# Performance work log

Hardware: AMD Instinct MI355X
Metric: run time of the kernel (lower is better)

The kernel has to match this reference:

```python
import jax, jax.numpy as jnp
import numpy as np

P = 512        # number of graph pairs
MAXN = 192     # max(len_s) by construction
D_IN = 32      # num_input_features
HID = 64       # hidden_dim
REG = 0.1      # entropic reg
ITERS = 8      # numItermax in forward call
DEG = 8        # avg degree for synthetic edges


def setup_inputs() -> dict:
    key = jax.random.key(0)
    ks = jax.random.split(key, 16)
    len_s = np.asarray(96 + (np.arange(P) % 97), dtype=np.int32)          # 96..192
    len_t = np.asarray(32 + ((np.arange(P) * 7) % 65), dtype=np.int32)    # 32..96 <= len_s
    Ns, Nt = int(len_s.sum()), int(len_t.sum())
    return {
        "x_s": jax.random.normal(ks[0], (Ns, D_IN), jnp.float32),
        "x_t": jax.random.normal(ks[1], (Nt, D_IN), jnp.float32),
        "W_rel0": 0.1 * jax.random.normal(ks[2], (D_IN, HID), jnp.float32),
        "b_rel0": 0.1 * jax.random.normal(ks[3], (HID,), jnp.float32),
        "W_root0": 0.1 * jax.random.normal(ks[4], (D_IN, HID), jnp.float32),
        "W_rel1": 0.1 * jax.random.normal(ks[5], (HID, HID), jnp.float32),
        "b_rel1": 0.1 * jax.random.normal(ks[6], (HID,), jnp.float32),
        "W_root1": 0.1 * jax.random.normal(ks[7], (HID, HID), jnp.float32),
        "W_e": 0.1 * jax.random.normal(ks[8], (D_IN + 2 * HID, 64), jnp.float32),
        "b_e": 0.1 * jax.random.normal(ks[9], (64,), jnp.float32),
        "virtual": jax.random.uniform(ks[10], (64,), jnp.float32),
        "edge_index_s": jax.random.randint(ks[11], (2, Ns * DEG), 0, Ns, dtype=jnp.int32),
        "edge_index_t": jax.random.randint(ks[12], (2, Nt * DEG), 0, Nt, dtype=jnp.int32),
        "len_s": jnp.asarray(len_s),
        "len_t": jnp.asarray(len_t),
    }


def _normalize(x):
    return x / jnp.clip(jnp.linalg.norm(x, axis=-1, keepdims=True), 1e-12)


def _gnn_embed(x, ei, layers, W_e, b_e):
    # GraphConv: out = lin_rel(sum_{j->i} x_j) + lin_root(x_i), then relu; cat all layer outputs
    outs = [x]
    h = x
    for (Wr, br, Wo) in layers:
        agg = jax.ops.segment_sum(h[ei[0]], ei[1], num_segments=h.shape[0])
        h = jax.nn.relu(agg @ Wr + br + h @ Wo)
        outs.append(h)
    emb = jnp.concatenate(outs, axis=1) @ W_e + b_e
    return _normalize(emb)


def _pad_gather(emb, lens):
    # [total, E] -> [P, MAXN, E] via per-pair offsets (indices clipped; invalid masked later)
    off = jnp.cumsum(lens) - lens
    idx = jnp.clip(off[:, None] + jnp.arange(MAXN)[None, :], 0, emb.shape[0] - 1)
    return emb[idx]


def reference(x_s, x_t, W_rel0, b_rel0, W_root0, W_rel1, b_rel1, W_root1,
              W_e, b_e, virtual, edge_index_s, edge_index_t, len_s, len_t):
    layers = [(W_rel0, b_rel0, W_root0), (W_rel1, b_rel1, W_root1)]
    emb_s = _gnn_embed(x_s, edge_index_s, layers, W_e, b_e)  # [Ns, 64]
    emb_t = _gnn_embed(x_t, edge_index_t, layers, W_e, b_e)  # [Nt, 64]
    virt = _normalize(virtual[None, :])[0]

    s_pad = _pad_gather(emb_s, len_s)  # [P, MAXN, 64]
    t_pad = _pad_gather(emb_t, len_t)  # [P, MAXN, 64]
    j = jnp.arange(MAXN)
    # columns >= len_t use the virtual node embedding (covers j in [m, n))
    t_mask = (j[None, :] < len_t[:, None])[:, :, None]
    t_aug = jnp.where(t_mask, t_pad, virt[None, None, :])

    # Euclidean cdist via quadratic expansion
    sq_s = jnp.sum(s_pad * s_pad, -1)                              # [P, MAXN]
    sq_t = jnp.sum(t_aug * t_aug, -1)                              # [P, MAXN]
    dot = jnp.einsum('pid,pjd->pij', s_pad, t_aug)                 # [P, MAXN, MAXN]
    cd = jnp.sqrt(jnp.maximum(sq_s[:, :, None] + sq_t[:, None, :] - 2.0 * dot, 1e-12))

    # padded cost: real block = cdist, bottom-right pad block = 0, rest = 1000
    row_valid = j[None, :] < len_s[:, None]                        # [P, MAXN] (n = len_s)
    in_block = row_valid[:, :, None] & row_valid[:, None, :]
    pad_block = (~row_valid)[:, :, None] & (~row_valid)[:, None, :]
    cost = jnp.where(in_block, cd, jnp.where(pad_block, 0.0, 1000.0))

    # Sinkhorn-Knopp, a = b = ones(MAXN) so Kp = K and updates are 1/(K v), 1/(K^T u)
    K = jnp.exp(-cost / REG)

    def body(_, uv):
        u, v = uv
        v = 1.0 / jnp.einsum('pij,pi->pj', K, u)
        u = 1.0 / jnp.einsum('pij,pj->pi', K, v)
        return (u, v)

    u0 = jnp.full((P, MAXN), 1.0 / MAXN, dtype=cost.dtype)
    u, v = jax.lax.fori_loop(0, ITERS, body, (u0, u0))
    gamma = jax.lax.stop_gradient(u[:, :, None] * K * v[:, None, :])

    geds = jnp.sum(gamma * cost, axis=(1, 2))
    geds2 = geds / (len_s + len_t).astype(cost.dtype)
    return gamma, cost, geds2
```

## Files before the change

kernel.cpp:

```cpp
#include <hip/hip_runtime.h>
#include <math.h>

#define PAIRS 512
#define MAXN 192

#define LDS_BAR() asm volatile("s_waitcnt lgkmcnt(0)\n\ts_barrier" ::: "memory")

__global__ void offsets_kernel(const int* __restrict__ ls, const int* __restrict__ lt,
                               int* __restrict__ off) {
    __shared__ int wa[8], wb[8];
    int t = threadIdx.x;
    int a = ls[t], b = lt[t];
    int ia = a, ib = b;
#pragma unroll
    for (int d = 1; d < 64; d <<= 1) {
        int xa = __shfl_up(ia, d, 64);
        int xb = __shfl_up(ib, d, 64);
        if ((t & 63) >= d) { ia += xa; ib += xb; }
    }
    if ((t & 63) == 63) { wa[t >> 6] = ia; wb[t >> 6] = ib; }
    __syncthreads();
    int pa = 0, pb = 0;
    for (int w = 0; w < (t >> 6); w++) { pa += wa[w]; pb += wb[w]; }
    off[t] = pa + ia - a;
    off[PAIRS + t] = pb + ib - b;
}

__global__ __launch_bounds__(256) void count2_kernel(const int* __restrict__ eiS,
                                                     const int* __restrict__ eiT,
                                                     int* __restrict__ cnt,
                                                     int Es, int Et, int split) {
    int e = blockIdx.x * 256 + threadIdx.x;
    if (e < Es) atomicAdd(&cnt[eiS[Es + e]], 1);
    else if (e < Es + Et) atomicAdd(&cnt[split + eiT[Et + (e - Es)]], 1);
}

__global__ __launch_bounds__(256) void scan1_kernel(int* __restrict__ data,
                                                    int* __restrict__ blockSums, int N) {
    __shared__ int sc[256];
    int t = threadIdx.x;
    int base = blockIdx.x * 1024;
    int v[4];
    int s = 0;
#pragma unroll
    for (int q = 0; q < 4; q++) {
        int i = base + t * 4 + q;
        v[q] = (i < N) ? data[i] : 0;
        s += v[q];
    }
    sc[t] = s;
    __syncthreads();
    for (int d = 1; d < 256; d <<= 1) {
        int x = (t >= d) ? sc[t - d] : 0;
        __syncthreads();
        sc[t] += x;
        __syncthreads();
    }
    int excl = sc[t] - s;
#pragma unroll
    for (int q = 0; q < 4; q++) {
        int i = base + t * 4 + q;
        if (i < N) { data[i] = excl; excl += v[q]; }
    }
    if (t == 255) blockSums[blockIdx.x] = sc[255];
}

__global__ void scan2_kernel(int* __restrict__ blockSums, int B) {
    __shared__ int sh[256];
    int t = threadIdx.x;
    int v = (t < B) ? blockSums[t] : 0;
    sh[t] = v;
    __syncthreads();
    for (int d = 1; d < 256; d <<= 1) {
        int x = (t >= d) ? sh[t - d] : 0;
        __syncthreads();
        sh[t] += x;
        __syncthreads();
    }
    if (t < B) blockSums[t] = sh[t] - v;
}

__global__ __launch_bounds__(256) void scan3_kernel(int* __restrict__ data,
                                                    const int* __restrict__ blockSums,
                                                    int* __restrict__ cursor, int N) {
    int i = blockIdx.x * 256 + threadIdx.x;
    if (i < N) {
        int v = data[i] + blockSums[i >> 10];
        data[i] = v;
        cursor[i] = v;
    }
}

__global__ __launch_bounds__(256) void fill2_kernel(const int* __restrict__ eiS,
                                                    const int* __restrict__ eiT,
                                                    int* __restrict__ cursor,
                                                    int* __restrict__ src,
                                                    int Es, int Et, int split) {
    int e = blockIdx.x * 256 + threadIdx.x;
    if (e < Es) {
        int p = atomicAdd(&cursor[eiS[Es + e]], 1);
        src[p] = eiS[e];
    } else if (e < Es + Et) {
        int ee = e - Es;
        int p = atomicAdd(&cursor[split + eiT[Et + ee]], 1);
        src[p] = eiT[ee];
    }
}

template <int F>
__global__ __launch_bounds__(256) void gather_kernel(const float* __restrict__ featA,
                                                     const float* __restrict__ featB,
                                                     int split,
                                                     const int* __restrict__ rs,
                                                     const int* __restrict__ re,
                                                     const int* __restrict__ src,
                                                     float* __restrict__ agg, int N) {
    int gid = blockIdx.x * 256 + threadIdx.x;
    int row = gid / F;
    int lane = threadIdx.x & (F - 1);
    if (row >= N) return;
    int b = rs[row], e = re[row];
    int cnt = e - b;
    const float* feat = (row < split) ? featA : featB;
    int pre = cnt < F ? cnt : F;
    int sidx = (lane < cnt) ? src[b + lane] : 0;
    float acc = 0.f;
    for (int q = 0; q < pre; q++) {
        int s = __shfl(sidx, q, F);
        acc += feat[(size_t)s * F + lane];
    }
    for (int q = b + F; q < e; q++) acc += feat[(size_t)src[q] * F + lane];
    agg[(size_t)row * F + lane] = acc;
}


#define FMA_ROW(r, av)                                     \
    acc[r][0] = fmaf(av.x, w0.x, acc[r][0]);               \
    acc[r][1] = fmaf(av.x, w0.y, acc[r][1]);               \
    acc[r][2] = fmaf(av.x, w0.z, acc[r][2]);               \
    acc[r][3] = fmaf(av.x, w0.w, acc[r][3]);               \
    acc[r][0] = fmaf(av.y, w1.x, acc[r][0]);               \
    acc[r][1] = fmaf(av.y, w1.y, acc[r][1]);               \
    acc[r][2] = fmaf(av.y, w1.z, acc[r][2]);               \
    acc[r][3] = fmaf(av.y, w1.w, acc[r][3]);               \
    acc[r][0] = fmaf(av.z, w2.x, acc[r][0]);               \
    acc[r][1] = fmaf(av.z, w2.y, acc[r][1]);               \
    acc[r][2] = fmaf(av.z, w2.z, acc[r][2]);               \
    acc[r][3] = fmaf(av.z, w2.w, acc[r][3]);               \
    acc[r][0] = fmaf(av.w, w3.x, acc[r][0]);               \
    acc[r][1] = fmaf(av.w, w3.y, acc[r][1]);               \
    acc[r][2] = fmaf(av.w, w3.z, acc[r][2]);               \
    acc[r][3] = fmaf(av.w, w3.w, acc[r][3]);

#define GEMM_INNER(KW4, AKP, WBP)                                          \
    _Pragma("unroll") for (int k4 = 0; k4 < (KW4); k4++) {                 \
        float4 a0 = *(const float4*)((AKP) + (i)      * 68 + 4 * k4);      \
        float4 a1 = *(const float4*)((AKP) + (i + 16) * 68 + 4 * k4);      \
        float4 a2 = *(const float4*)((AKP) + (i + 32) * 68 + 4 * k4);      \
        float4 a3 = *(const float4*)((AKP) + (i + 48) * 68 + 4 * k4);      \
        float4 w0 = (WBP)[(4 * k4 + 0) * 16 + j];                          \
        float4 w1 = (WBP)[(4 * k4 + 1) * 16 + j];                          \
        float4 w2 = (WBP)[(4 * k4 + 2) * 16 + j];                          \
        float4 w3 = (WBP)[(4 * k4 + 3) * 16 + j];                          \
        FMA_ROW(0, a0) FMA_ROW(1, a1) FMA_ROW(2, a2) FMA_ROW(3, a3)        \
    }

template <int KIN>
__global__ __launch_bounds__(256) void lin_gemm_kernel(const float* __restrict__ agg,
    const float* __restrict__ hinA, const float* __restrict__ hinB, int split,
    const float* __restrict__ Wrel, const float* __restrict__ brel,
    const float* __restrict__ Wroot, float* __restrict__ hout, int N) {
    __shared__ float Abuf[64 * 68];
    __shared__ float4 Wbuf[64 * 16];
    int tid = threadIdx.x;
    int i = tid & 15, j = tid >> 4;
    int rowbase = blockIdx.x * 64;
    float4 bv = ((const float4*)brel)[j];
    float acc[4][4];
#pragma unroll
    for (int r = 0; r < 4; r++) { acc[r][0] = bv.x; acc[r][1] = bv.y; acc[r][2] = bv.z; acc[r][3] = bv.w; }

    for (int c0 = 0; c0 < 2 * KIN; c0 += 64) {
        __syncthreads();
        for (int t = tid; t < 1024; t += 256) {
            int k4 = t & 15, r = t >> 4;
            int kg = c0 + 4 * k4;
            int row = rowbase + r; if (row >= N) row = N - 1;
            float4 v;
            if (kg < KIN) {
                v = ((const float4*)(agg + (size_t)row * KIN))[kg >> 2];
            } else {
                int kk = kg - KIN;
                const float* h = (row < split) ? hinA + (size_t)row * KIN
                                               : hinB + (size_t)(row - split) * KIN;
                v = ((const float4*)h)[kk >> 2];
            }
            *(float4*)(Abuf + r * 68 + 4 * k4) = v;
        }
        for (int t = tid; t < 1024; t += 256) {
            int k = t >> 4, jj = t & 15;
            int kg = c0 + k;
            const float* Wsrc = (kg < KIN) ? (Wrel + (size_t)kg * 64)
                                           : (Wroot + (size_t)(kg - KIN) * 64);
            Wbuf[t] = ((const float4*)Wsrc)[jj];
        }
        __syncthreads();
        GEMM_INNER(16, Abuf, Wbuf)
    }
#pragma unroll
    for (int r = 0; r < 4; r++) {
        int row = rowbase + i + 16 * r;
        if (row < N) {
            float4 o = make_float4(fmaxf(acc[r][0], 0.f), fmaxf(acc[r][1], 0.f),
                                   fmaxf(acc[r][2], 0.f), fmaxf(acc[r][3], 0.f));
            ((float4*)(hout + (size_t)row * 64))[j] = o;
        }
    }
}

__global__ __launch_bounds__(256) void lin64_emb_kernel(
    const float* __restrict__ agg, const float* __restrict__ h1,
    const float* __restrict__ xA, const float* __restrict__ xB, int split,
    const float* __restrict__ Wrel, const float* __restrict__ brel,
    const float* __restrict__ Wroot,
    const float* __restrict__ We, const float* __restrict__ be,
    float* __restrict__ emb, int N) {
    __shared__ float Abuf[64 * 68];
    __shared__ float4 Wbuf[64 * 16];
    __shared__ float h2buf[64 * 68];
    int tid = threadIdx.x;
    int i = tid & 15, j = tid >> 4;
    int rowbase = blockIdx.x * 64;

    {
        float4 bv = ((const float4*)brel)[j];
        float acc[4][4];
#pragma unroll
        for (int r = 0; r < 4; r++) { acc[r][0] = bv.x; acc[r][1] = bv.y; acc[r][2] = bv.z; acc[r][3] = bv.w; }

        for (int c0 = 0; c0 < 128; c0 += 64) {
            __syncthreads();
            for (int t = tid; t < 1024; t += 256) {
                int k4 = t & 15, r = t >> 4;
                int kg = c0 + 4 * k4;
                int row = rowbase + r; if (row >= N) row = N - 1;
                float4 v;
                if (kg < 64) v = ((const float4*)(agg + (size_t)row * 64))[kg >> 2];
                else         v = ((const float4*)(h1 + (size_t)row * 64))[(kg - 64) >> 2];
                *(float4*)(Abuf + r * 68 + 4 * k4) = v;
            }
            for (int t = tid; t < 1024; t += 256) {
                int k = t >> 4, jj = t & 15;
                int kg = c0 + k;
                const float* Wsrc = (kg < 64) ? (Wrel + (size_t)kg * 64)
                                              : (Wroot + (size_t)(kg - 64) * 64);
                Wbuf[t] = ((const float4*)Wsrc)[jj];
            }
            __syncthreads();
            GEMM_INNER(16, Abuf, Wbuf)
        }
#pragma unroll
        for (int r = 0; r < 4; r++) {
            float4 o = make_float4(fmaxf(acc[r][0], 0.f), fmaxf(acc[r][1], 0.f),
                                   fmaxf(acc[r][2], 0.f), fmaxf(acc[r][3], 0.f));
            *(float4*)(h2buf + (i + 16 * r) * 68 + 4 * j) = o;
        }
    }

    float4 bv = ((const float4*)be)[j];
    float acc[4][4];
#pragma unroll
    for (int r = 0; r < 4; r++) { acc[r][0] = bv.x; acc[r][1] = bv.y; acc[r][2] = bv.z; acc[r][3] = bv.w; }

    __syncthreads();
    for (int t = tid; t < 1024; t += 256) {
        int k4 = t & 15, r = t >> 4;
        int kg = 4 * k4;
        int row = rowbase + r; if (row >= N) row = N - 1;
        float4 v;
        if (kg < 32) {
            const float* x = (row < split) ? xA + (size_t)row * 32
                                           : xB + (size_t)(row - split) * 32;
            v = ((const float4*)x)[kg >> 2];
        } else {
            v = ((const float4*)(h1 + (size_t)row * 64))[(kg - 32) >> 2];
        }
        *(float4*)(Abuf + r * 68 + 4 * k4) = v;
    }
    for (int t = tid; t < 1024; t += 256) {
        int k = t >> 4, jj = t & 15;
        Wbuf[t] = ((const float4*)(We + (size_t)k * 64))[jj];
    }
    __syncthreads();
    GEMM_INNER(16, Abuf, Wbuf)

    __syncthreads();
    for (int t = tid; t < 512; t += 256) {
        int k4 = t & 7, r = t >> 3;
        int row = rowbase + r; if (row >= N) row = N - 1;
        float4 v = ((const float4*)(h1 + (size_t)row * 64))[8 + k4];
        *(float4*)(Abuf + r * 68 + 4 * k4) = v;
    }
    for (int t = tid; t < 512; t += 256) {
        int k = t >> 4, jj = t & 15;
        Wbuf[t] = ((const float4*)(We + (size_t)(64 + k) * 64))[jj];
    }
    __syncthreads();
    GEMM_INNER(8, Abuf, Wbuf)

    __syncthreads();
    for (int t = tid; t < 1024; t += 256) {
        int k = t >> 4, jj = t & 15;
        Wbuf[t] = ((const float4*)(We + (size_t)(96 + k) * 64))[jj];
    }
    __syncthreads();
    GEMM_INNER(16, h2buf, Wbuf)

    __syncthreads();
#pragma unroll
    for (int r = 0; r < 4; r++)
#pragma unroll
        for (int c = 0; c < 4; c++)
            Abuf[(i + 16 * r) * 68 + 4 * j + c] = acc[r][c];
    __syncthreads();
    int lane = tid & 63, wv = tid >> 6;
    for (int rr = 0; rr < 16; rr++) {
        int r = wv * 16 + rr;
        float val = Abuf[r * 68 + lane];
        float ss = val * val;
#pragma unroll
        for (int d = 32; d > 0; d >>= 1) ss += __shfl_xor(ss, d, 64);
        int row = rowbase + r;
        if (row < N) emb[(size_t)row * 64 + lane] = val / fmaxf(sqrtf(ss), 1e-12f);
    }
}

__device__ __forceinline__ void dot_half(float kh[3][12], const float* sS, const float* sT,
                                         int ti, int tj) {
#pragma unroll
    for (int s = 0; s < 3; s++)
#pragma unroll
        for (int b = 0; b < 12; b++) kh[s][b] = 0.f;
    for (int k4 = 0; k4 < 16; k4++) {
        float4 a0 = *(const float4*)(sS + (3 * ti + 0) * 68 + 4 * k4);
        float4 a1 = *(const float4*)(sS + (3 * ti + 1) * 68 + 4 * k4);
        float4 a2 = *(const float4*)(sS + (3 * ti + 2) * 68 + 4 * k4);
#pragma unroll
        for (int b = 0; b < 12; b++) {
            float4 tb = *(const float4*)(sT + (12 * tj + b) * 68 + 4 * k4);
            kh[0][b] = fmaf(a0.x, tb.x, kh[0][b]);
            kh[0][b] = fmaf(a0.y, tb.y, kh[0][b]);
            kh[0][b] = fmaf(a0.z, tb.z, kh[0][b]);
            kh[0][b] = fmaf(a0.w, tb.w, kh[0][b]);
            kh[1][b] = fmaf(a1.x, tb.x, kh[1][b]);
            kh[1][b] = fmaf(a1.y, tb.y, kh[1][b]);
            kh[1][b] = fmaf(a1.z, tb.z, kh[1][b]);
            kh[1][b] = fmaf(a1.w, tb.w, kh[1][b]);
            kh[2][b] = fmaf(a2.x, tb.x, kh[2][b]);
            kh[2][b] = fmaf(a2.y, tb.y, kh[2][b]);
            kh[2][b] = fmaf(a2.z, tb.z, kh[2][b]);
            kh[2][b] = fmaf(a2.w, tb.w, kh[2][b]);
        }
    }
}

__device__ __forceinline__ void epi_half(float kh[3][12], const float* sqS, const float* sqT,
                                         int h, int ti, int tj, int n, int p,
                                         float* __restrict__ cost_out) {
#pragma unroll
    for (int s = 0; s < 3; s++) {
        int i = 96 * h + 3 * ti + s;
        bool rv = i < n;
        float sqi = sqS[3 * ti + s];
        float tmp[12];
#pragma unroll
        for (int b = 0; b < 12; b++) {
            int j = 12 * tj + b;
            float cd = sqrtf(fmaxf(sqi + sqT[j] - 2.f * kh[s][b], 1e-12f));
            float c = (rv && (j < n)) ? cd : ((!rv && (j >= n)) ? 0.f : 1000.f);
            tmp[b] = c;
            kh[s][b] = __expf(-10.f * c);
        }
        float* orow = cost_out + ((size_t)p * MAXN + i) * MAXN + 12 * tj;
#pragma unroll
        for (int q = 0; q < 3; q++)
            ((float4*)orow)[q] = make_float4(tmp[4 * q], tmp[4 * q + 1],
                                             tmp[4 * q + 2], tmp[4 * q + 3]);
    }
}

__global__ __launch_bounds__(512, 4) void fused_cost_sinkhorn_kernel(
    const float* __restrict__ embS, const float* __restrict__ embT,
    const float* __restrict__ vraw,
    const int* __restrict__ lenS, const int* __restrict__ lenT,
    const int* __restrict__ off,
    float* __restrict__ cost_out, float* __restrict__ gamma_out,
    float* __restrict__ geds2, int Ns) {
    __shared__ __align__(16) float sT[192 * 68];
    __shared__ __align__(16) float sS[96 * 68];
    __shared__ __align__(16) float sqT[192];
    __shared__ __align__(16) float sqS[96];
    __shared__ __align__(16) float virtv[64];

    int p = blockIdx.x;
    int tid = threadIdx.x;
    int ti = tid & 31;
    int tj = tid >> 5;
    int n = lenS[p], m = lenT[p];
    int offs = off[p], offt = off[PAIRS + p];

    if (tid < 64) {
        float v = vraw[tid];
        float ss = v * v;
#pragma unroll
        for (int d = 32; d > 0; d >>= 1) ss += __shfl_xor(ss, d, 64);
        virtv[tid] = v / fmaxf(sqrtf(ss), 1e-12f);
    }
    __syncthreads();

    for (int t = tid; t < 192 * 16; t += 512) {
        int j = t >> 4, q = t & 15;
        float4 vv = (j < m) ? ((const float4*)embT)[(size_t)(offt + j) * 16 + q]
                            : ((const float4*)virtv)[q];
        *(float4*)(sT + j * 68 + 4 * q) = vv;
    }
    for (int t = tid; t < 96 * 16; t += 512) {
        int r = t >> 4, q = t & 15;
        int gi = offs + r; if (gi > Ns - 1) gi = Ns - 1;
        float4 vv = ((const float4*)embS)[(size_t)gi * 16 + q];
        *(float4*)(sS + r * 68 + 4 * q) = vv;
    }
    __syncthreads();
    if (tid < 192) {
        float s = 0.f;
#pragma unroll
        for (int k = 0; k < 64; k++) { float a = sT[tid * 68 + k]; s = fmaf(a, a, s); }
        sqT[tid] = s;
    } else if (tid < 288) {
        int r = tid - 192;
        float s = 0.f;
#pragma unroll
        for (int k = 0; k < 64; k++) { float a = sS[r * 68 + k]; s = fmaf(a, a, s); }
        sqS[r] = s;
    }
    __syncthreads();

    float kf[2][3][12];

    dot_half(kf[0], sS, sT, ti, tj);
    float4 pf0, pf1, pf2;
    {
        int t0 = tid, t1 = tid + 512, t2 = tid + 1024;
        int gi0 = offs + 96 + (t0 >> 4); if (gi0 > Ns - 1) gi0 = Ns - 1;
        int gi1 = offs + 96 + (t1 >> 4); if (gi1 > Ns - 1) gi1 = Ns - 1;
        int gi2 = offs + 96 + (t2 >> 4); if (gi2 > Ns - 1) gi2 = Ns - 1;
        pf0 = ((const float4*)embS)[(size_t)gi0 * 16 + (t0 & 15)];
        pf1 = ((const float4*)embS)[(size_t)gi1 * 16 + (t1 & 15)];
        pf2 = ((const float4*)embS)[(size_t)gi2 * 16 + (t2 & 15)];
    }
    epi_half(kf[0], sqS, sqT, 0, ti, tj, n, p, cost_out);

    LDS_BAR();
    {
        int t0 = tid, t1 = tid + 512, t2 = tid + 1024;
        *(float4*)(sS + (t0 >> 4) * 68 + 4 * (t0 & 15)) = pf0;
        *(float4*)(sS + (t1 >> 4) * 68 + 4 * (t1 & 15)) = pf1;
        *(float4*)(sS + (t2 >> 4) * 68 + 4 * (t2 & 15)) = pf2;
    }
    LDS_BAR();
    if (tid < 96) {
        float s = 0.f;
#pragma unroll
        for (int k = 0; k < 64; k++) { float a = sS[tid * 68 + k]; s = fmaf(a, a, s); }
        sqS[tid] = s;
    }
    LDS_BAR();

    dot_half(kf[1], sS, sT, ti, tj);
    epi_half(kf[1], sqS, sqT, 1, ti, tj, n, p, cost_out);
    LDS_BAR();

    float* part = sS;
    float* ubuf = sS + 6336;
    float* vbuf = sqT;

    if (tid < 192) ubuf[tid] = 1.f / 192.f;
    LDS_BAR();

    for (int it = 0; it < 8; it++) {
        float uloc[6];
#pragma unroll
        for (int h = 0; h < 2; h++)
#pragma unroll
            for (int s = 0; s < 3; s++) uloc[3 * h + s] = ubuf[96 * h + 3 * ti + s];
#pragma unroll
        for (int b = 0; b < 12; b++) {
            float a = 0.f;
#pragma unroll
            for (int h = 0; h < 2; h++)
#pragma unroll
                for (int s = 0; s < 3; s++) a = fmaf(kf[h][s][b], uloc[3 * h + s], a);
            part[(12 * tj + b) * 33 + ti] = a;
        }
        LDS_BAR();
        if (tid < 192) {
            float s = 0.f;
#pragma unroll
            for (int g = 0; g < 32; g++) s += part[tid * 33 + g];
            vbuf[tid] = 1.f / s;
        }
        LDS_BAR();
        float vloc[12];
        {
            float4 va = *(const float4*)(vbuf + 12 * tj);
            float4 vb = *(const float4*)(vbuf + 12 * tj + 4);
            float4 vc = *(const float4*)(vbuf + 12 * tj + 8);
            vloc[0] = va.x; vloc[1] = va.y; vloc[2] = va.z; vloc[3] = va.w;
            vloc[4] = vb.x; vloc[5] = vb.y; vloc[6] = vb.z; vloc[7] = vb.w;
            vloc[8] = vc.x; vloc[9] = vc.y; vloc[10] = vc.z; vloc[11] = vc.w;
        }
#pragma unroll
        for (int h = 0; h < 2; h++)
#pragma unroll
            for (int s = 0; s < 3; s++) {
                float a = 0.f;
#pragma unroll
                for (int b = 0; b < 12; b++) a = fmaf(kf[h][s][b], vloc[b], a);
                part[tj * 192 + 96 * h + 3 * ti + s] = a;
            }
        LDS_BAR();
        if (tid < 192) {
            float s = 0.f;
#pragma unroll
            for (int g = 0; g < 16; g++) s += part[g * 192 + tid];
            ubuf[tid] = 1.f / s;
        }
        LDS_BAR();
    }

    float vloc[12];
    {
        float4 va = *(const float4*)(vbuf + 12 * tj);
        float4 vb = *(const float4*)(vbuf + 12 * tj + 4);
        float4 vc = *(const float4*)(vbuf + 12 * tj + 8);
        vloc[0] = va.x; vloc[1] = va.y; vloc[2] = va.z; vloc[3] = va.w;
        vloc[4] = vb.x; vloc[5] = vb.y; vloc[6] = vb.z; vloc[7] = vb.w;
        vloc[8] = vc.x; vloc[9] = vc.y; vloc[10] = vc.z; vloc[11] = vc.w;
    }
    float accg = 0.f;
#pragma unroll
    for (int h = 0; h < 2; h++)
#pragma unroll
        for (int s = 0; s < 3; s++) {
            int i = 96 * h + 3 * ti + s;
            float ui = ubuf[i];
            float tmp[12];
#pragma unroll
            for (int b = 0; b < 12; b++) {
                float Kij = kf[h][s][b];
                float gg = ui * Kij * vloc[b];
                tmp[b] = gg;
                if (Kij > 0.f) accg = fmaf(gg, -0.1f * __logf(Kij), accg);
            }
            float* grow = gamma_out + ((size_t)p * MAXN + i) * MAXN + 12 * tj;
#pragma unroll
            for (int q = 0; q < 3; q++)
                ((float4*)grow)[q] = make_float4(tmp[4 * q], tmp[4 * q + 1],
                                                 tmp[4 * q + 2], tmp[4 * q + 3]);
        }
#pragma unroll
    for (int d = 32; d > 0; d >>= 1) accg += __shfl_xor(accg, d, 64);
    if ((tid & 63) == 0) sqS[tid >> 6] = accg;
    LDS_BAR();
    if (tid == 0) {
        float s = 0.f;
        for (int w = 0; w < 8; w++) s += sqS[w];
        geds2[p] = s / (float)(n + m);
    }
}

extern "C" void kernel_launch(void* const* d_in, const int* in_sizes, int n_in,
                              void* d_out, int out_size, void* d_ws, size_t ws_size,
                              hipStream_t stream) {
    const float* x_s     = (const float*)d_in[0];
    const float* x_t     = (const float*)d_in[1];
    const float* W_rel0  = (const float*)d_in[2];
    const float* b_rel0  = (const float*)d_in[3];
    const float* W_root0 = (const float*)d_in[4];
    const float* W_rel1  = (const float*)d_in[5];
    const float* b_rel1  = (const float*)d_in[6];
    const float* W_root1 = (const float*)d_in[7];
    const float* W_e     = (const float*)d_in[8];
    const float* b_e     = (const float*)d_in[9];
    const float* virt    = (const float*)d_in[10];
    const int*   ei_s    = (const int*)d_in[11];
    const int*   ei_t    = (const int*)d_in[12];
    const int*   len_s   = (const int*)d_in[13];
    const int*   len_t   = (const int*)d_in[14];

    int Ns = in_sizes[0] / 32;
    int Nt = in_sizes[1] / 32;
    int Es = in_sizes[11] / 2;
    int Et = in_sizes[12] / 2;
    int Ntot = Ns + Nt;
    int Etot = Es + Et;

    char* w = (char*)d_ws;
    int* off  = (int*)w;              w += 1024 * 4;
    int* bsum = (int*)w;              w += 256 * 4;
    int* rs   = (int*)w;              w += (size_t)Ntot * 4;
    int* cur  = (int*)w;              w += (size_t)Ntot * 4;
    int* src  = (int*)w;              w += (size_t)Etot * 4;
    w = (char*)(((size_t)w + 255) & ~(size_t)255);
    float* agg = (float*)w;           w += (size_t)Ntot * 64 * 4;
    float* h1  = (float*)w;           w += (size_t)Ntot * 64 * 4;

    float* out_gamma = (float*)d_out;
    float* out_cost  = out_gamma + (size_t)PAIRS * MAXN * MAXN;
    float* out_geds  = out_cost + (size_t)PAIRS * MAXN * MAXN;

    offsets_kernel<<<1, PAIRS, 0, stream>>>(len_s, len_t, off);

    hipMemsetAsync(rs, 0, (size_t)Ntot * 4, stream);
    count2_kernel<<<(Etot + 255) / 256, 256, 0, stream>>>(ei_s, ei_t, rs, Es, Et, Ns);
    int nb = (Ntot + 1023) / 1024;
    scan1_kernel<<<nb, 256, 0, stream>>>(rs, bsum, Ntot);
    scan2_kernel<<<1, 256, 0, stream>>>(bsum, nb);
    scan3_kernel<<<(Ntot + 255) / 256, 256, 0, stream>>>(rs, bsum, cur, Ntot);
    fill2_kernel<<<(Etot + 255) / 256, 256, 0, stream>>>(ei_s, ei_t, cur, src, Es, Et, Ns);

    int gblk = (Ntot + 63) / 64;

    gather_kernel<32><<<(int)(((long long)Ntot * 32 + 255) / 256), 256, 0, stream>>>(
        x_s, x_t, Ns, rs, cur, src, agg, Ntot);
    lin_gemm_kernel<32><<<gblk, 256, 0, stream>>>(
        agg, x_s, x_t, Ns, W_rel0, b_rel0, W_root0, h1, Ntot);
    gather_kernel<64><<<(int)(((long long)Ntot * 64 + 255) / 256), 256, 0, stream>>>(
        h1, h1, Ns, rs, cur, src, agg, Ntot);
    lin64_emb_kernel<<<gblk, 256, 0, stream>>>(
        agg, h1, x_s, x_t, Ns, W_rel1, b_rel1, W_root1, W_e, b_e, agg, Ntot);

    fused_cost_sinkhorn_kernel<<<PAIRS, 512, 0, stream>>>(
        agg, agg + (size_t)Ns * 64, virt, len_s, len_t, off,
        out_cost, out_gamma, out_geds, Ns);
}
```

Before: 578.4 us.

## Stage gamma and cost stores through LDS for coalesced row writes

Cost output is no longer written during the epilogue. Both gamma and cost are now staged in LDS in 64-row chunks and written out as contiguous full rows, so global stores are coalesced instead of scattered 48-byte pieces per thread. Cost values for the valid block are recomputed from K via -0.1*log(K) rather than kept from the original cdist. This adds several barriers and LDS round trips, and the log can underflow when K is zero for large distances, changing cost values.

Result: slower. 710.7 us (+22.9%).

```diff
diff --git a/kernel.cpp b/kernel.cpp
--- a/kernel.cpp
+++ b/kernel.cpp
@@ -365,27 +365,19 @@
 }
 
 __device__ __forceinline__ void epi_half(float kh[3][12], const float* sqS, const float* sqT,
-                                         int h, int ti, int tj, int n, int p,
-                                         float* __restrict__ cost_out) {
+                                         int h, int ti, int tj, int n) {
 #pragma unroll
     for (int s = 0; s < 3; s++) {
         int i = 96 * h + 3 * ti + s;
         bool rv = i < n;
         float sqi = sqS[3 * ti + s];
-        float tmp[12];
 #pragma unroll
         for (int b = 0; b < 12; b++) {
             int j = 12 * tj + b;
             float cd = sqrtf(fmaxf(sqi + sqT[j] - 2.f * kh[s][b], 1e-12f));
             float c = (rv && (j < n)) ? cd : ((!rv && (j >= n)) ? 0.f : 1000.f);
-            tmp[b] = c;
             kh[s][b] = __expf(-10.f * c);
         }
-        float* orow = cost_out + ((size_t)p * MAXN + i) * MAXN + 12 * tj;
-#pragma unroll
-        for (int q = 0; q < 3; q++)
-            ((float4*)orow)[q] = make_float4(tmp[4 * q], tmp[4 * q + 1],
-                                             tmp[4 * q + 2], tmp[4 * q + 3]);
     }
 }
 
@@ -458,7 +450,7 @@
         pf1 = ((const float4*)embS)[(size_t)gi1 * 16 + (t1 & 15)];
         pf2 = ((const float4*)embS)[(size_t)gi2 * 16 + (t2 & 15)];
     }
-    epi_half(kf[0], sqS, sqT, 0, ti, tj, n, p, cost_out);
+    epi_half(kf[0], sqS, sqT, 0, ti, tj, n);
 
     LDS_BAR();
     {
@@ -477,7 +469,7 @@
     LDS_BAR();
 
     dot_half(kf[1], sS, sT, ti, tj);
-    epi_half(kf[1], sqS, sqT, 1, ti, tj, n, p, cost_out);
+    epi_half(kf[1], sqS, sqT, 1, ti, tj, n);
     LDS_BAR();
 
     float* part = sS;
@@ -547,27 +539,82 @@
         vloc[4] = vb.x; vloc[5] = vb.y; vloc[6] = vb.z; vloc[7] = vb.w;
         vloc[8] = vc.x; vloc[9] = vc.y; vloc[10] = vc.z; vloc[11] = vc.w;
     }
+    float* stg = sT;
+    int crow = tid >> 3, c8 = tid & 7;
     float accg = 0.f;
-#pragma unroll
-    for (int h = 0; h < 2; h++)
-#pragma unroll
-        for (int s = 0; s < 3; s++) {
-            int i = 96 * h + 3 * ti + s;
-            float ui = ubuf[i];
-            float tmp[12];
-#pragma unroll
-            for (int b = 0; b < 12; b++) {
-                float Kij = kf[h][s][b];
-                float gg = ui * Kij * vloc[b];
-                tmp[b] = gg;
-                if (Kij > 0.f) accg = fmaf(gg, -0.1f * __logf(Kij), accg);
-            }
-            float* grow = gamma_out + ((size_t)p * MAXN + i) * MAXN + 12 * tj;
-#pragma unroll
-            for (int q = 0; q < 3; q++)
-                ((float4*)grow)[q] = make_float4(tmp[4 * q], tmp[4 * q + 1],
-                                                 tmp[4 * q + 2], tmp[4 * q + 3]);
-        }
+
+    for (int c = 0; c < 3; c++) {
+#pragma unroll
+        for (int h = 0; h < 2; h++)
+#pragma unroll
+            for (int s = 0; s < 3; s++) {
+                int i = 96 * h + 3 * ti + s;
+                int r = i - 64 * c;
+                if (r >= 0 && r < 64) {
+                    float ui = ubuf[i];
+                    float tmp[12];
+#pragma unroll
+                    for (int b = 0; b < 12; b++) {
+                        float Kij = kf[h][s][b];
+                        float gg = ui * Kij * vloc[b];
+                        tmp[b] = gg;
+                        if (Kij > 0.f) accg = fmaf(gg, -0.1f * __logf(Kij), accg);
+                    }
+                    float* d = stg + r * 200 + 12 * tj;
+#pragma unroll
+                    for (int q = 0; q < 3; q++)
+                        ((float4*)d)[q] = make_float4(tmp[4 * q], tmp[4 * q + 1],
+                                                      tmp[4 * q + 2], tmp[4 * q + 3]);
+                }
+            }
+        LDS_BAR();
+        {
+            float* gb = gamma_out + ((size_t)p * MAXN + 64 * c + crow) * MAXN;
+#pragma unroll
+            for (int q = 0; q < 6; q++) {
+                int col4 = c8 + 8 * q;
+                float4 vv = *(const float4*)(stg + crow * 200 + 4 * col4);
+                ((float4*)gb)[col4] = vv;
+            }
+        }
+        LDS_BAR();
+#pragma unroll
+        for (int h = 0; h < 2; h++)
+#pragma unroll
+            for (int s = 0; s < 3; s++) {
+                int i = 96 * h + 3 * ti + s;
+                int r = i - 64 * c;
+                if (r >= 0 && r < 64) {
+                    bool rv = i < n;
+                    float tmp[12];
+#pragma unroll
+                    for (int b = 0; b < 12; b++) {
+                        int jj = 12 * tj + b;
+                        float cc;
+                        if (rv && (jj < n)) cc = -0.1f * __logf(kf[h][s][b]);
+                        else cc = (!rv && (jj >= n)) ? 0.f : 1000.f;
+                        tmp[b] = cc;
+                    }
+                    float* d = stg + r * 200 + 12 * tj;
+#pragma unroll
+                    for (int q = 0; q < 3; q++)
+                        ((float4*)d)[q] = make_float4(tmp[4 * q], tmp[4 * q + 1],
+                                                      tmp[4 * q + 2], tmp[4 * q + 3]);
+                }
+            }
+        LDS_BAR();
+        {
+            float* cb = cost_out + ((size_t)p * MAXN + 64 * c + crow) * MAXN;
+#pragma unroll
+            for (int q = 0; q < 6; q++) {
+                int col4 = c8 + 8 * q;
+                float4 vv = *(const float4*)(stg + crow * 200 + 4 * col4);
+                ((float4*)cb)[col4] = vv;
+            }
+        }
+        LDS_BAR();
+    }
+
 #pragma unroll
     for (int d = 32; d > 0; d >>= 1) accg += __shfl_xor(accg, d, 64);
     if ((tid & 63) == 0) sqS[tid >> 6] = accg;
```
